# Kernel optimization log

Measured on AMD Instinct MI355X. Metric: run time of the kernel, lower is better.

Reference implementation:

```python
import jax, jax.numpy as jnp
import numpy as np

H = 16  # num_heads (matches init_kwargs)
MASK_VAL = -10000.0


def setup_inputs() -> dict:
    key = jax.random.key(0)
    k1, k2, k3, k4, k5 = jax.random.split(key, 5)
    B, N, C = 2, 2048, 1024
    hidden_states = jax.random.normal(k1, (B, N, C), dtype=jnp.float32)
    encoder_hidden_states = jax.random.normal(k2, (B, N, C), dtype=jnp.float32)
    pad_mask = jax.random.bernoulli(k3, 0.1, (B, N))
    # Linear weights stored as (in, out); scaled ~Xavier so softmax isn't saturated
    W_q = jax.random.normal(k4, (C, C), dtype=jnp.float32) * (C ** -0.5)
    W_c = jax.random.normal(k5, (C, 2 * C), dtype=jnp.float32) * (C ** -0.5)
    return {"hidden_states": hidden_states,
            "encoder_hidden_states": encoder_hidden_states,
            "pad_mask": pad_mask,
            "W_q": W_q,
            "W_c": W_c}


def _split_heads(x, B, N, C):
    # (B, N, C) -> (B, H, N, D)
    return x.reshape(B, N, H, C // H).transpose(0, 2, 1, 3)


def reference(hidden_states, encoder_hidden_states, pad_mask, W_q, W_c):
    B, N, C = hidden_states.shape
    D = C // H
    scaler = D ** -0.5

    q = hidden_states @ W_q                       # (B, N, C)
    kv = encoder_hidden_states @ W_c              # (B, N, 2C)
    k, v = kv[..., :C], kv[..., C:]

    q = _split_heads(q, B, N, C)                  # (B, H, N, D)
    k = _split_heads(k, B, N, C)
    v = _split_heads(v, B, N, C)

    scores = jnp.einsum('bhid,bhjd->bhij', q, k) * scaler  # (B, H, N, N)

    # construct_mask: expanded[b,i,j] = pad_mask[b,i] OR pad_mask[b,j]
    expanded = pad_mask[:, None, :, None] | pad_mask[:, None, None, :]
    scores = jnp.where(expanded, MASK_VAL, scores)

    # max-subtract + softmax (dropout_rate=0 so dropout is identity)
    scores = scores - jax.lax.stop_gradient(scores.max(axis=-1, keepdims=True))
    att_weights = jax.nn.softmax(scores, axis=-1)

    att = jnp.einsum('bhij,bhjd->bhid', att_weights, v)   # (B, H, N, D)
    att = att.transpose(0, 2, 1, 3).reshape(B, N, C)
    return att, att_weights
```

## Files before the change

### kernel.cpp

```cpp
#include <hip/hip_runtime.h>
#include <math.h>

#define B_ 2
#define N_ 2048
#define C_ 1024
#define H_ 16
#define D_ 64

typedef __attribute__((ext_vector_type(8))) short short8v;
typedef __attribute__((ext_vector_type(4))) short short4v;
typedef __attribute__((ext_vector_type(4))) float f32x4;

static __device__ __forceinline__ short f2bf(float f) {
    union { float f; unsigned u; } v; v.f = f;
    unsigned r = v.u + 0x7FFFu + ((v.u >> 16) & 1u);
    return (short)(r >> 16);
}

static __device__ __forceinline__ void splitbf(float f, short& h, short& l) {
    union { float f; unsigned u; } v; v.f = f;
    const unsigned uh = v.u & 0xFFFF0000u;
    h = (short)(uh >> 16);
    union { unsigned u; float f; } w; w.u = uh;
    union { float f; unsigned u; } x; x.f = f - w.f;
    l = (short)(x.u >> 16);
}

#define GKSTR 40

__global__ __launch_bounds__(256) void gemm_x3(const float* __restrict__ A,
                                               const float* __restrict__ Bm,
                                               short* __restrict__ Cm,
                                               int K, int N) {
    __shared__ __align__(16) short Ahi[128][GKSTR];
    __shared__ __align__(16) short Alo[128][GKSTR];
    __shared__ __align__(16) short Bhi[64][GKSTR];
    __shared__ __align__(16) short Blo[64][GKSTR];

    const int t  = threadIdx.x;
    const int w  = t >> 6;
    const int l  = t & 63;
    const int lq = l & 15;
    const int hq = l >> 4;
    const int wr = w >> 1;
    const int wc = w & 1;
    const int m0 = blockIdx.y * 128;
    const int n0 = blockIdx.x * 64;

    const int arow = t >> 3;
    const int akc  = (t & 7) * 4;
    const int bn   = t & 63;
    const int bkq  = w * 8;

    f32x4 acc[4][2];
#pragma unroll
    for (int mi = 0; mi < 4; ++mi)
#pragma unroll
        for (int ni = 0; ni < 2; ++ni) acc[mi][ni] = (f32x4){0.f, 0.f, 0.f, 0.f};

    float4 af[4];
    float  bf[8];
#pragma unroll
    for (int it = 0; it < 4; ++it)
        af[it] = *(const float4*)&A[(size_t)(m0 + arow + it * 32) * K + akc];
#pragma unroll
    for (int kk = 0; kk < 8; ++kk)
        bf[kk] = Bm[(size_t)(bkq + kk) * N + n0 + bn];

    short4v ah[4], al[4];
    short8v bh, bl;
#pragma unroll
    for (int it = 0; it < 4; ++it) {
        short h, lo2;
        splitbf(af[it].x, h, lo2); ah[it][0] = h; al[it][0] = lo2;
        splitbf(af[it].y, h, lo2); ah[it][1] = h; al[it][1] = lo2;
        splitbf(af[it].z, h, lo2); ah[it][2] = h; al[it][2] = lo2;
        splitbf(af[it].w, h, lo2); ah[it][3] = h; al[it][3] = lo2;
    }
#pragma unroll
    for (int kk = 0; kk < 8; ++kk) {
        short h, lo2;
        splitbf(bf[kk], h, lo2); bh[kk] = h; bl[kk] = lo2;
    }

    for (int k0 = 0; k0 < K; k0 += 32) {
        __syncthreads();
#pragma unroll
        for (int it = 0; it < 4; ++it) {
            *(short4v*)&Ahi[arow + it * 32][akc] = ah[it];
            *(short4v*)&Alo[arow + it * 32][akc] = al[it];
        }
        *(short8v*)&Bhi[bn][bkq] = bh;
        *(short8v*)&Blo[bn][bkq] = bl;
        __syncthreads();

        const int kn = k0 + 32;
        if (kn < K) {
#pragma unroll
            for (int it = 0; it < 4; ++it)
                af[it] = *(const float4*)&A[(size_t)(m0 + arow + it * 32) * K + kn + akc];
#pragma unroll
            for (int kk = 0; kk < 8; ++kk)
                bf[kk] = Bm[(size_t)(kn + bkq + kk) * N + n0 + bn];
        }

        short8v amh[4], aml[4], bnh[2], bnl[2];
#pragma unroll
        for (int mi = 0; mi < 4; ++mi) {
            amh[mi] = *(const short8v*)&Ahi[wr * 64 + mi * 16 + lq][hq * 8];
            aml[mi] = *(const short8v*)&Alo[wr * 64 + mi * 16 + lq][hq * 8];
        }
#pragma unroll
        for (int ni = 0; ni < 2; ++ni) {
            bnh[ni] = *(const short8v*)&Bhi[wc * 32 + ni * 16 + lq][hq * 8];
            bnl[ni] = *(const short8v*)&Blo[wc * 32 + ni * 16 + lq][hq * 8];
        }
#pragma unroll
        for (int mi = 0; mi < 4; ++mi)
#pragma unroll
            for (int ni = 0; ni < 2; ++ni) {
                acc[mi][ni] = __builtin_amdgcn_mfma_f32_16x16x32_bf16(amh[mi], bnh[ni], acc[mi][ni], 0, 0, 0);
                acc[mi][ni] = __builtin_amdgcn_mfma_f32_16x16x32_bf16(amh[mi], bnl[ni], acc[mi][ni], 0, 0, 0);
                acc[mi][ni] = __builtin_amdgcn_mfma_f32_16x16x32_bf16(aml[mi], bnh[ni], acc[mi][ni], 0, 0, 0);
            }

        if (kn < K) {
#pragma unroll
            for (int it = 0; it < 4; ++it) {
                short h, lo2;
                splitbf(af[it].x, h, lo2); ah[it][0] = h; al[it][0] = lo2;
                splitbf(af[it].y, h, lo2); ah[it][1] = h; al[it][1] = lo2;
                splitbf(af[it].z, h, lo2); ah[it][2] = h; al[it][2] = lo2;
                splitbf(af[it].w, h, lo2); ah[it][3] = h; al[it][3] = lo2;
            }
#pragma unroll
            for (int kk = 0; kk < 8; ++kk) {
                short h, lo2;
                splitbf(bf[kk], h, lo2); bh[kk] = h; bl[kk] = lo2;
            }
        }
    }

#pragma unroll
    for (int mi = 0; mi < 4; ++mi)
#pragma unroll
        for (int ni = 0; ni < 2; ++ni) {
            const int col = n0 + wc * 32 + ni * 16 + lq;
#pragma unroll
            for (int r = 0; r < 4; ++r) {
                const int row = m0 + wr * 64 + mi * 16 + hq * 4 + r;
                Cm[(size_t)row * N + col] = f2bf(acc[mi][ni][r]);
            }
        }
}

__global__ __launch_bounds__(256) void v_transpose(const short* __restrict__ kv_bf,
                                                   short* __restrict__ vt) {
    __shared__ __align__(16) short Ls[128][72];
    const int t  = threadIdx.x;
    const int jt = blockIdx.x * 128;
    const int h  = blockIdx.y;
    const int b  = blockIdx.z;
    const short* src = kv_bf + (size_t)b * N_ * 2 * C_ + C_ + h * D_;
#pragma unroll
    for (int it = 0; it < 4; ++it) {
        const int idx = it * 256 + t;
        const int j = idx >> 3, d0 = (idx & 7) * 8;
        *(short8v*)&Ls[j][d0] = *(const short8v*)&src[(size_t)(jt + j) * (2 * C_) + d0];
    }
    __syncthreads();
    short* dst = vt + ((size_t)(b * H_ + h)) * D_ * N_;
#pragma unroll
    for (int it = 0; it < 4; ++it) {
        const int idx = it * 256 + t;
        const int d  = idx >> 4;
        const int j0 = (idx & 15) * 8;
        short8v s;
#pragma unroll
        for (int jj = 0; jj < 8; ++jj) s[jj] = Ls[j0 + jj][d];
        *(short8v*)&dst[(size_t)d * N_ + jt + j0] = s;
    }
}

#define KSTR 72
#define VSTR 136
#define PSTR 136

__global__ __launch_bounds__(256) void attn_mfma(const short* __restrict__ q,
                                                 const short* __restrict__ kv,
                                                 const short* __restrict__ vtg,
                                                 const int* __restrict__ mask,
                                                 float* __restrict__ out_att,
                                                 float* __restrict__ out_w) {
    __shared__ __align__(16) short Ks[128][KSTR];
    __shared__ __align__(16) short Vt[64][VSTR];
    __shared__ __align__(16) short Ps[4][32][PSTR];
    __shared__ float linv_s[4][32];
    __shared__ int   mcol_s[128];

    const int t  = threadIdx.x;
    const int w  = t >> 6;
    const int l  = t & 63;
    const int lq = l & 15;
    const int hq = l >> 4;

    const int lin = blockIdx.x;
    const int swz = (lin & 7) * 64 + (lin >> 3);
    const int qb = swz & 15;
    const int h  = (swz >> 4) & 15;
    const int b  = swz >> 8;
    const int i0 = qb * 128 + w * 32;

    const int sj = t >> 3;
    const int sd = (t & 7) * 8;
    const int vd = t >> 4;
    const int vj = (t & 15) * 8;

    short8v qa[2][2];
#pragma unroll
    for (int g = 0; g < 2; ++g) {
        const short* qrow = q + ((size_t)(b * N_ + i0 + g * 16 + lq)) * C_ + h * D_;
        qa[g][0] = *(const short8v*)&qrow[hq * 8];
        qa[g][1] = *(const short8v*)&qrow[32 + hq * 8];
    }

    int mr[2][4];
#pragma unroll
    for (int g = 0; g < 2; ++g)
#pragma unroll
        for (int r = 0; r < 4; ++r) mr[g][r] = mask[b * N_ + i0 + g * 16 + hq * 4 + r];

    const short* kbase = kv + (size_t)b * N_ * 2 * C_ + h * D_;
    const short* vtb   = vtg + ((size_t)(b * H_ + h)) * D_ * N_;

    float lsum[2][4];
#pragma unroll
    for (int g = 0; g < 2; ++g)
#pragma unroll
        for (int r = 0; r < 4; ++r) lsum[g][r] = 0.f;

    short8v kr[4];
    int mpre = 0;
#pragma unroll
    for (int it = 0; it < 4; ++it)
        kr[it] = *(const short8v*)&kbase[(size_t)(it * 32 + sj) * (2 * C_) + sd];
    if (t < 128) mpre = mask[b * N_ + t];

    for (int tile = 0; tile < 16; ++tile) {
        __syncthreads();
#pragma unroll
        for (int it = 0; it < 4; ++it)
            *(short8v*)&Ks[it * 32 + sj][sd] = kr[it];
        if (t < 128) mcol_s[t] = mpre;
        __syncthreads();

        if (tile < 15) {
            const int jn = (tile + 1) * 128;
#pragma unroll
            for (int it = 0; it < 4; ++it)
                kr[it] = *(const short8v*)&kbase[(size_t)(jn + it * 32 + sj) * (2 * C_) + sd];
            if (t < 128) mpre = mask[b * N_ + jn + t];
        }

#pragma unroll
        for (int cb = 0; cb < 8; ++cb) {
            const short8v b0 = *(short8v*)&Ks[cb * 16 + lq][hq * 8];
            const short8v b1 = *(short8v*)&Ks[cb * 16 + lq][32 + hq * 8];
            const int mc = mcol_s[cb * 16 + lq];
#pragma unroll
            for (int g = 0; g < 2; ++g) {
                f32x4 acc = {0.f, 0.f, 0.f, 0.f};
                acc = __builtin_amdgcn_mfma_f32_16x16x32_bf16(qa[g][0], b0, acc, 0, 0, 0);
                acc = __builtin_amdgcn_mfma_f32_16x16x32_bf16(qa[g][1], b1, acc, 0, 0, 0);
#pragma unroll
                for (int r = 0; r < 4; ++r)
                    lsum[g][r] += mr[g][r] ? 1.0f : (mc ? 0.0f : __expf(acc[r] * 0.125f));
            }
        }
    }
    float inv[2][4];
#pragma unroll
    for (int g = 0; g < 2; ++g)
#pragma unroll
        for (int r = 0; r < 4; ++r) {
            float s = lsum[g][r];
#pragma unroll
            for (int off = 1; off < 16; off <<= 1) s += __shfl_xor(s, off, 64);
            inv[g][r] = 1.0f / s;
        }
    if (lq == 0)
#pragma unroll
        for (int g = 0; g < 2; ++g)
#pragma unroll
            for (int r = 0; r < 4; ++r) linv_s[w][g * 16 + hq * 4 + r] = inv[g][r];

    float* wbase[2];
#pragma unroll
    for (int g = 0; g < 2; ++g)
        wbase[g] = out_w + ((size_t)((b * H_ + h) * N_ + i0 + g * 16 + hq * 4)) * N_;

    f32x4 oacc[4][2];
#pragma unroll
    for (int db = 0; db < 4; ++db)
#pragma unroll
        for (int g = 0; g < 2; ++g) oacc[db][g] = (f32x4){0.f, 0.f, 0.f, 0.f};

    short8v vr[4];
#pragma unroll
    for (int it = 0; it < 4; ++it) {
        kr[it] = *(const short8v*)&kbase[(size_t)(it * 32 + sj) * (2 * C_) + sd];
        vr[it] = *(const short8v*)&vtb[(size_t)(it * 16 + vd) * N_ + vj];
    }
    if (t < 128) mpre = mask[b * N_ + t];

    for (int tile = 0; tile < 16; ++tile) {
        const int jt = tile * 128;
        __syncthreads();
#pragma unroll
        for (int it = 0; it < 4; ++it) {
            *(short8v*)&Ks[it * 32 + sj][sd] = kr[it];
            *(short8v*)&Vt[it * 16 + vd][vj] = vr[it];
        }
        if (t < 128) mcol_s[t] = mpre;
        __syncthreads();

        if (tile < 15) {
            const int jn = jt + 128;
#pragma unroll
            for (int it = 0; it < 4; ++it) {
                kr[it] = *(const short8v*)&kbase[(size_t)(jn + it * 32 + sj) * (2 * C_) + sd];
                vr[it] = *(const short8v*)&vtb[(size_t)(it * 16 + vd) * N_ + jn + vj];
            }
            if (t < 128) mpre = mask[b * N_ + jn + t];
        }

#pragma unroll
        for (int cb = 0; cb < 8; ++cb) {
            const short8v b0 = *(short8v*)&Ks[cb * 16 + lq][hq * 8];
            const short8v b1 = *(short8v*)&Ks[cb * 16 + lq][32 + hq * 8];
            const int mc   = mcol_s[cb * 16 + lq];
            const int jcol = cb * 16 + lq;
#pragma unroll
            for (int g = 0; g < 2; ++g) {
                f32x4 acc = {0.f, 0.f, 0.f, 0.f};
                acc = __builtin_amdgcn_mfma_f32_16x16x32_bf16(qa[g][0], b0, acc, 0, 0, 0);
                acc = __builtin_amdgcn_mfma_f32_16x16x32_bf16(qa[g][1], b1, acc, 0, 0, 0);
#pragma unroll
                for (int r = 0; r < 4; ++r) {
                    const float ev = mr[g][r] ? 1.0f : (mc ? 0.0f : __expf(acc[r] * 0.125f));
                    wbase[g][(size_t)r * N_ + jt + jcol] = ev * inv[g][r];
                    Ps[w][g * 16 + hq * 4 + r][jcol] = f2bf(ev);
                }
            }
        }
        __syncthreads();

        short8v pb[2][4];
#pragma unroll
        for (int kb = 0; kb < 4; ++kb) {
            pb[0][kb] = *(short8v*)&Ps[w][lq][kb * 32 + hq * 8];
            pb[1][kb] = *(short8v*)&Ps[w][16 + lq][kb * 32 + hq * 8];
        }
#pragma unroll
        for (int db = 0; db < 4; ++db)
#pragma unroll
            for (int kb = 0; kb < 4; ++kb) {
                const short8v va = *(short8v*)&Vt[db * 16 + lq][kb * 32 + hq * 8];
                oacc[db][0] = __builtin_amdgcn_mfma_f32_16x16x32_bf16(va, pb[0][kb], oacc[db][0], 0, 0, 0);
                oacc[db][1] = __builtin_amdgcn_mfma_f32_16x16x32_bf16(va, pb[1][kb], oacc[db][1], 0, 0, 0);
            }
    }

#pragma unroll
    for (int g = 0; g < 2; ++g) {
        const float invi = linv_s[w][g * 16 + lq];
        const size_t abase = ((size_t)(b * N_ + i0 + g * 16 + lq)) * C_ + h * D_;
#pragma unroll
        for (int db = 0; db < 4; ++db)
#pragma unroll
            for (int r = 0; r < 4; ++r)
                out_att[abase + db * 16 + hq * 4 + r] = oacc[db][g][r] * invi;
    }
}

extern "C" void kernel_launch(void* const* d_in, const int* in_sizes, int n_in,
                              void* d_out, int out_size, void* d_ws, size_t ws_size,
                              hipStream_t stream) {
    const float* hs   = (const float*)d_in[0];
    const float* ehs  = (const float*)d_in[1];
    const int*   mask = (const int*)d_in[2];
    const float* W_q  = (const float*)d_in[3];
    const float* W_c  = (const float*)d_in[4];

    float* out_att = (float*)d_out;
    float* out_w   = (float*)d_out + (size_t)B_ * N_ * C_;

    short* qbf  = (short*)d_ws;
    short* kvbf = qbf + (size_t)B_ * N_ * C_;
    short* vt   = kvbf + (size_t)B_ * N_ * 2 * C_;

    gemm_x3<<<dim3(C_ / 64, (B_ * N_) / 128), 256, 0, stream>>>(
        hs, W_q, qbf, C_, C_);
    gemm_x3<<<dim3((2 * C_) / 64, (B_ * N_) / 128), 256, 0, stream>>>(
        ehs, W_c, kvbf, C_, 2 * C_);
    v_transpose<<<dim3(N_ / 128, H_, B_), 256, 0, stream>>>(kvbf, vt);

    attn_mfma<<<dim3(512), 256, 0, stream>>>(
        qbf, kvbf, vt, mask, out_att, out_w);
}
```

Before: 321.5 us.

## Pre-split inputs into bf16 hi/lo planes and enlarge GEMM tile to 128x128

Moves the fp32-to-bf16 hi/lo splitting out of the GEMM inner loop into separate pre-pass kernels. The weight split also transposes it to K-major so both operands load as contiguous 16-byte vectors. The GEMM tile grows from 128x64 to 128x128, so each block issues more MFMAs per shared-memory load. The trade-off is extra launches and extra global traffic for the split planes, plus workspace reuse: vt aliases the Ah buffer.

```diff
diff --git a/kernel.cpp b/kernel.cpp
--- a/kernel.cpp
+++ b/kernel.cpp
@@ -26,117 +26,129 @@
     l = (short)(x.u >> 16);
 }
 
+__global__ __launch_bounds__(256) void split_a(const float* __restrict__ src,
+                                               short* __restrict__ hi,
+                                               short* __restrict__ lo) {
+    const int i = (blockIdx.x * 256 + threadIdx.x) * 4;
+    const float4 f = *(const float4*)&src[i];
+    short4v h, l;
+    short th_, tl_;
+    splitbf(f.x, th_, tl_); h[0] = th_; l[0] = tl_;
+    splitbf(f.y, th_, tl_); h[1] = th_; l[1] = tl_;
+    splitbf(f.z, th_, tl_); h[2] = th_; l[2] = tl_;
+    splitbf(f.w, th_, tl_); h[3] = th_; l[3] = tl_;
+    *(short4v*)&hi[i] = h;
+    *(short4v*)&lo[i] = l;
+}
+
+__global__ __launch_bounds__(256) void split_wt(const float* __restrict__ Wm,
+                                                short* __restrict__ th,
+                                                short* __restrict__ tl,
+                                                int K, int N) {
+    __shared__ float Ls[64][68];
+    const int t  = threadIdx.x;
+    const int n0 = blockIdx.x * 64;
+    const int k0 = blockIdx.y * 64;
+#pragma unroll
+    for (int it = 0; it < 4; ++it) {
+        const int kl = it * 16 + (t >> 4);
+        const int nl = (t & 15) * 4;
+        *(float4*)&Ls[kl][nl] = *(const float4*)&Wm[(size_t)(k0 + kl) * N + n0 + nl];
+    }
+    __syncthreads();
+#pragma unroll
+    for (int it = 0; it < 4; ++it) {
+        const int idx = it * 256 + t;
+        const int nl  = idx & 63;
+        const int ks  = (idx >> 6) * 4;
+        short4v h, l;
+#pragma unroll
+        for (int j = 0; j < 4; ++j) {
+            short th_, tl_;
+            splitbf(Ls[ks + j][nl], th_, tl_);
+            h[j] = th_; l[j] = tl_;
+        }
+        *(short4v*)&th[(size_t)(n0 + nl) * K + k0 + ks] = h;
+        *(short4v*)&tl[(size_t)(n0 + nl) * K + k0 + ks] = l;
+    }
+}
+
 #define GKSTR 40
 
-__global__ __launch_bounds__(256) void gemm_x3(const float* __restrict__ A,
-                                               const float* __restrict__ Bm,
-                                               short* __restrict__ Cm,
-                                               int K, int N) {
-    __shared__ __align__(16) short Ahi[128][GKSTR];
-    __shared__ __align__(16) short Alo[128][GKSTR];
-    __shared__ __align__(16) short Bhi[64][GKSTR];
-    __shared__ __align__(16) short Blo[64][GKSTR];
+__global__ __launch_bounds__(256) void gemm_bf3(const short* __restrict__ Ah,
+                                                const short* __restrict__ Al,
+                                                const short* __restrict__ Bth,
+                                                const short* __restrict__ Btl,
+                                                short* __restrict__ Cm,
+                                                int K, int N) {
+    __shared__ __align__(16) short Ahs[128][GKSTR];
+    __shared__ __align__(16) short Als[128][GKSTR];
+    __shared__ __align__(16) short Bhs[128][GKSTR];
+    __shared__ __align__(16) short Bls[128][GKSTR];
 
     const int t  = threadIdx.x;
     const int w  = t >> 6;
-    const int l  = t & 63;
-    const int lq = l & 15;
-    const int hq = l >> 4;
+    const int lq = t & 15;
+    const int hq = (t & 63) >> 4;
     const int wr = w >> 1;
     const int wc = w & 1;
     const int m0 = blockIdx.y * 128;
-    const int n0 = blockIdx.x * 64;
-
-    const int arow = t >> 3;
-    const int akc  = (t & 7) * 4;
-    const int bn   = t & 63;
-    const int bkq  = w * 8;
-
-    f32x4 acc[4][2];
+    const int n0 = blockIdx.x * 128;
+
+    const int srow = t >> 1;
+    const int scol = (t & 1) * 16;
+
+    const short* gA_h = &Ah[(size_t)(m0 + srow) * K + scol];
+    const short* gA_l = &Al[(size_t)(m0 + srow) * K + scol];
+    const short* gB_h = &Bth[(size_t)(n0 + srow) * K + scol];
+    const short* gB_l = &Btl[(size_t)(n0 + srow) * K + scol];
+
+    f32x4 acc[4][4];
 #pragma unroll
     for (int mi = 0; mi < 4; ++mi)
 #pragma unroll
-        for (int ni = 0; ni < 2; ++ni) acc[mi][ni] = (f32x4){0.f, 0.f, 0.f, 0.f};
-
-    float4 af[4];
-    float  bf[8];
-#pragma unroll
-    for (int it = 0; it < 4; ++it)
-        af[it] = *(const float4*)&A[(size_t)(m0 + arow + it * 32) * K + akc];
-#pragma unroll
-    for (int kk = 0; kk < 8; ++kk)
-        bf[kk] = Bm[(size_t)(bkq + kk) * N + n0 + bn];
-
-    short4v ah[4], al[4];
-    short8v bh, bl;
-#pragma unroll
-    for (int it = 0; it < 4; ++it) {
-        short h, lo2;
-        splitbf(af[it].x, h, lo2); ah[it][0] = h; al[it][0] = lo2;
-        splitbf(af[it].y, h, lo2); ah[it][1] = h; al[it][1] = lo2;
-        splitbf(af[it].z, h, lo2); ah[it][2] = h; al[it][2] = lo2;
-        splitbf(af[it].w, h, lo2); ah[it][3] = h; al[it][3] = lo2;
-    }
-#pragma unroll
-    for (int kk = 0; kk < 8; ++kk) {
-        short h, lo2;
-        splitbf(bf[kk], h, lo2); bh[kk] = h; bl[kk] = lo2;
-    }
+        for (int ni = 0; ni < 4; ++ni) acc[mi][ni] = (f32x4){0.f, 0.f, 0.f, 0.f};
+
+    short8v ra_h0 = *(const short8v*)gA_h,       ra_h1 = *(const short8v*)(gA_h + 8);
+    short8v ra_l0 = *(const short8v*)gA_l,       ra_l1 = *(const short8v*)(gA_l + 8);
+    short8v rb_h0 = *(const short8v*)gB_h,       rb_h1 = *(const short8v*)(gB_h + 8);
+    short8v rb_l0 = *(const short8v*)gB_l,       rb_l1 = *(const short8v*)(gB_l + 8);
 
     for (int k0 = 0; k0 < K; k0 += 32) {
         __syncthreads();
-#pragma unroll
-        for (int it = 0; it < 4; ++it) {
-            *(short4v*)&Ahi[arow + it * 32][akc] = ah[it];
-            *(short4v*)&Alo[arow + it * 32][akc] = al[it];
-        }
-        *(short8v*)&Bhi[bn][bkq] = bh;
-        *(short8v*)&Blo[bn][bkq] = bl;
+        *(short8v*)&Ahs[srow][scol]     = ra_h0;
+        *(short8v*)&Ahs[srow][scol + 8] = ra_h1;
+        *(short8v*)&Als[srow][scol]     = ra_l0;
+        *(short8v*)&Als[srow][scol + 8] = ra_l1;
+        *(short8v*)&Bhs[srow][scol]     = rb_h0;
+        *(short8v*)&Bhs[srow][scol + 8] = rb_h1;
+        *(short8v*)&Bls[srow][scol]     = rb_l0;
+        *(short8v*)&Bls[srow][scol + 8] = rb_l1;
         __syncthreads();
 
         const int kn = k0 + 32;
         if (kn < K) {
-#pragma unroll
-            for (int it = 0; it < 4; ++it)
-                af[it] = *(const float4*)&A[(size_t)(m0 + arow + it * 32) * K + kn + akc];
-#pragma unroll
-            for (int kk = 0; kk < 8; ++kk)
-                bf[kk] = Bm[(size_t)(kn + bkq + kk) * N + n0 + bn];
-        }
-
-        short8v amh[4], aml[4], bnh[2], bnl[2];
+            ra_h0 = *(const short8v*)(gA_h + kn); ra_h1 = *(const short8v*)(gA_h + kn + 8);
+            ra_l0 = *(const short8v*)(gA_l + kn); ra_l1 = *(const short8v*)(gA_l + kn + 8);
+            rb_h0 = *(const short8v*)(gB_h + kn); rb_h1 = *(const short8v*)(gB_h + kn + 8);
+            rb_l0 = *(const short8v*)(gB_l + kn); rb_l1 = *(const short8v*)(gB_l + kn + 8);
+        }
+
+        short8v bnh[4], bnl[4];
+#pragma unroll
+        for (int ni = 0; ni < 4; ++ni) {
+            bnh[ni] = *(const short8v*)&Bhs[wc * 64 + ni * 16 + lq][hq * 8];
+            bnl[ni] = *(const short8v*)&Bls[wc * 64 + ni * 16 + lq][hq * 8];
+        }
 #pragma unroll
         for (int mi = 0; mi < 4; ++mi) {
-            amh[mi] = *(const short8v*)&Ahi[wr * 64 + mi * 16 + lq][hq * 8];
-            aml[mi] = *(const short8v*)&Alo[wr * 64 + mi * 16 + lq][hq * 8];
-        }
-#pragma unroll
-        for (int ni = 0; ni < 2; ++ni) {
-            bnh[ni] = *(const short8v*)&Bhi[wc * 32 + ni * 16 + lq][hq * 8];
-            bnl[ni] = *(const short8v*)&Blo[wc * 32 + ni * 16 + lq][hq * 8];
-        }
-#pragma unroll
-        for (int mi = 0; mi < 4; ++mi)
-#pragma unroll
-            for (int ni = 0; ni < 2; ++ni) {
-                acc[mi][ni] = __builtin_amdgcn_mfma_f32_16x16x32_bf16(amh[mi], bnh[ni], acc[mi][ni], 0, 0, 0);
-                acc[mi][ni] = __builtin_amdgcn_mfma_f32_16x16x32_bf16(amh[mi], bnl[ni], acc[mi][ni], 0, 0, 0);
-                acc[mi][ni] = __builtin_amdgcn_mfma_f32_16x16x32_bf16(aml[mi], bnh[ni], acc[mi][ni], 0, 0, 0);
-            }
-
-        if (kn < K) {
-#pragma unroll
-            for (int it = 0; it < 4; ++it) {
-                short h, lo2;
-                splitbf(af[it].x, h, lo2); ah[it][0] = h; al[it][0] = lo2;
-                splitbf(af[it].y, h, lo2); ah[it][1] = h; al[it][1] = lo2;
-                splitbf(af[it].z, h, lo2); ah[it][2] = h; al[it][2] = lo2;
-                splitbf(af[it].w, h, lo2); ah[it][3] = h; al[it][3] = lo2;
-            }
-#pragma unroll
-            for (int kk = 0; kk < 8; ++kk) {
-                short h, lo2;
-                splitbf(bf[kk], h, lo2); bh[kk] = h; bl[kk] = lo2;
+            const short8v amh = *(const short8v*)&Ahs[wr * 64 + mi * 16 + lq][hq * 8];
+            const short8v aml = *(const short8v*)&Als[wr * 64 + mi * 16 + lq][hq * 8];
+#pragma unroll
+            for (int ni = 0; ni < 4; ++ni) {
+                acc[mi][ni] = __builtin_amdgcn_mfma_f32_16x16x32_bf16(amh, bnh[ni], acc[mi][ni], 0, 0, 0);
+                acc[mi][ni] = __builtin_amdgcn_mfma_f32_16x16x32_bf16(amh, bnl[ni], acc[mi][ni], 0, 0, 0);
+                acc[mi][ni] = __builtin_amdgcn_mfma_f32_16x16x32_bf16(aml, bnh[ni], acc[mi][ni], 0, 0, 0);
             }
         }
     }
@@ -144,8 +156,8 @@
 #pragma unroll
     for (int mi = 0; mi < 4; ++mi)
 #pragma unroll
-        for (int ni = 0; ni < 2; ++ni) {
-            const int col = n0 + wc * 32 + ni * 16 + lq;
+        for (int ni = 0; ni < 4; ++ni) {
+            const int col = n0 + wc * 64 + ni * 16 + lq;
 #pragma unroll
             for (int r = 0; r < 4; ++r) {
                 const int row = m0 + wr * 64 + mi * 16 + hq * 4 + r;
@@ -395,16 +407,28 @@
     float* out_att = (float*)d_out;
     float* out_w   = (float*)d_out + (size_t)B_ * N_ * C_;
 
+    const size_t M1 = (size_t)1024 * 1024;
     short* qbf  = (short*)d_ws;
-    short* kvbf = qbf + (size_t)B_ * N_ * C_;
-    short* vt   = kvbf + (size_t)B_ * N_ * 2 * C_;
-
-    gemm_x3<<<dim3(C_ / 64, (B_ * N_) / 128), 256, 0, stream>>>(
-        hs, W_q, qbf, C_, C_);
-    gemm_x3<<<dim3((2 * C_) / 64, (B_ * N_) / 128), 256, 0, stream>>>(
-        ehs, W_c, kvbf, C_, 2 * C_);
+    short* kvbf = qbf + 4 * M1;
+    short* Ah   = kvbf + 8 * M1;
+    short* Al   = Ah + 4 * M1;
+    short* vt   = Ah;
+    short* Wth  = Al + 4 * M1;
+    short* Wtl  = Wth + 2 * M1;
+
+    const int nelems_a = B_ * N_ * C_;
+
+    split_a<<<dim3(nelems_a / 1024), 256, 0, stream>>>(hs, Ah, Al);
+    split_wt<<<dim3(C_ / 64, C_ / 64), 256, 0, stream>>>(W_q, Wth, Wtl, C_, C_);
+    gemm_bf3<<<dim3(C_ / 128, (B_ * N_) / 128), 256, 0, stream>>>(
+        Ah, Al, Wth, Wtl, qbf, C_, C_);
+
+    split_a<<<dim3(nelems_a / 1024), 256, 0, stream>>>(ehs, Ah, Al);
+    split_wt<<<dim3((2 * C_) / 64, C_ / 64), 256, 0, stream>>>(W_c, Wth, Wtl, C_, 2 * C_);
+    gemm_bf3<<<dim3((2 * C_) / 128, (B_ * N_) / 128), 256, 0, stream>>>(
+        Ah, Al, Wth, Wtl, kvbf, C_, 2 * C_);
+
     v_transpose<<<dim3(N_ / 128, H_, B_), 256, 0, stream>>>(kvbf, vt);
-
     attn_mfma<<<dim3(512), 256, 0, stream>>>(
         qbf, kvbf, vt, mask, out_att, out_w);
 }
```

Result: no change. 324.4 us (+0.9%).
